# Optimization experiments

Hardware: AMD Instinct MI355X
Metric: run time of the kernel (lower is better)

Reference implementation:

```python
import jax, jax.numpy as jnp
import numpy as np
from jax import lax

N, D, K, R, T = 200000, 128, 64, 4, 50000
L = 2 * R  # positive + negative relation layers
ITERATIONS = 2


def _l2norm(x, eps=1e-12):
    # torch F.normalize(p=2): x / max(||x||, eps)
    n = jnp.sqrt(jnp.sum(x * x, axis=-1, keepdims=True))
    return x / jnp.maximum(n, eps)


def setup_inputs() -> dict:
    key = jax.random.key(0)
    ks = jax.random.split(key, 8)
    # Unique write targets (a permutation) so the last-write scatter is deterministic;
    # matches input_specs' randint intent (indices uniform in [0, N)).
    perm = jax.random.permutation(ks[0], N)
    subj_idx = perm[:T].astype(jnp.int32)
    obj_idx = perm[T:2 * T].astype(jnp.int32)
    layer_idx = jax.random.randint(ks[1], (T,), 0, L, dtype=jnp.int32)
    memberships = jax.random.randint(ks[2], (N, K), 0, 2, dtype=jnp.int32)
    embedding_m = jax.random.normal(ks[3], (N, D), dtype=jnp.float32)
    # ClassUpdate params: [d+K] -> d
    Wc = jax.random.normal(ks[4], (D + K, D), dtype=jnp.float32) / np.sqrt(D + K)
    bc = jnp.zeros((D,), dtype=jnp.float32)
    # RelationUpdate params, one layer per (relation, polarity): [2d] -> [2d]
    Wr = jax.random.normal(ks[5], (L, 2 * D, 2 * D), dtype=jnp.float32) / np.sqrt(2 * D)
    br = jnp.zeros((L, 2 * D), dtype=jnp.float32)
    return {
        'embedding_m': embedding_m,
        'memberships': memberships,
        'subj_idx': subj_idx,
        'obj_idx': obj_idx,
        'layer_idx': layer_idx,
        'Wc': Wc, 'bc': bc, 'Wr': Wr, 'br': br,
    }


def reference(embedding_m, memberships, subj_idx, obj_idx, layer_idx, Wc, bc, Wr, br):
    mem = memberships.astype(embedding_m.dtype)  # [N, K]
    t_ar = jnp.arange(T)

    def iteration(e, _):
        # --- ClassUpdate: e' = l2norm(tanh([e; m] Wc + bc)) ---
        x = jnp.concatenate([e, mem], axis=1)           # [N, d+K]
        e = _l2norm(jnp.tanh(x @ Wc + bc))              # [N, d]
        # --- RelationUpdates: reads come from the post-class-update snapshot `e`
        pair = jnp.concatenate([e[subj_idx], e[obj_idx]], axis=1)   # [T, 2d]
        # compute through all L relation layers, then select each triple's layer
        out_all = jnp.einsum('tc,lcd->tld', pair, Wr) + br          # [T, L, 2d]
        out = jnp.tanh(out_all[t_ar, layer_idx])                    # [T, 2d]
        new_s = _l2norm(out[:, :D])
        new_o = _l2norm(out[:, D:])
        e_next = e.at[subj_idx].set(new_s).at[obj_idx].set(new_o)
        return e_next, None

    e_final, _ = lax.scan(iteration, embedding_m, None, length=ITERATIONS)
    return e_final
```

## Files before the change

kernel.cpp:

```cpp
#include <hip/hip_runtime.h>
#include <hip/hip_bf16.h>


#define NROWS 200000
#define DD    128
#define KK    64
#define TT    50000
#define LL    8
#define BT    64
#define PADT  50560
#define NPASS 3125

#define NB    100
#define CHB   500
#define PL    8
#define PREPB 268
#define MBB   6250

#define WS_OFFS   0
#define WS_CNT    64
#define WS_BASE   4096
#define WS_BINS   8192
#define WS_WCP    210432
#define WS_WRP    (WS_WCP + 6*8*64*16)
#define WS_MB     (WS_WRP + 8*8*16*64*16)
#define WS_E16    (WS_MB + NROWS*8)
#define WS_NEED   (WS_E16 + (size_t)NROWS*DD*2)

typedef unsigned short u16;
typedef unsigned int   u32;
typedef unsigned long long u64;
typedef unsigned char  u8;
typedef __attribute__((ext_vector_type(8))) short bf16x8;
typedef __attribute__((ext_vector_type(4))) float f32x4;
typedef __attribute__((ext_vector_type(4))) unsigned int u32x4;

#define SWZ(row, byte) ((byte) ^ (((row)&7)<<4))

__device__ __forceinline__ u32 bfbits(float f){
  __hip_bfloat16 h = __float2bfloat16(f);
  return (u32)*reinterpret_cast<unsigned short*>(&h);
}
__device__ __forceinline__ u32 pk(float lo, float hi){
  return bfbits(lo) | (bfbits(hi) << 16);
}
__device__ __forceinline__ float qreduce16(float ss){
  ss += __shfl_xor(ss, 1, 64);
  ss += __shfl_xor(ss, 2, 64);
  ss += __shfl_xor(ss, 4, 64);
  ss += __shfl_xor(ss, 8, 64);
  return ss;
}
__device__ __forceinline__ float fast_tanh(float x){
  float a = fabsf(x);
  float e = __expf(-2.0f*a);
  float t = (1.0f - e) * __builtin_amdgcn_rcpf(1.0f + e);
  return copysignf(t, x);
}
__device__ __forceinline__ float rnorm_scale(float ss){
  return __builtin_amdgcn_rcpf(fmaxf(__builtin_amdgcn_sqrtf(ss), 1e-12f));
}
__device__ __forceinline__ void nt_store_v4(void* p, u32x4 v){
  __builtin_nontemporal_store(v, (u32x4*)p);
}

__global__ __launch_bounds__(256) void k_prep(
    const float* __restrict__ Wc, const float* __restrict__ Wr,
    uint4* __restrict__ wcp, uint4* __restrict__ wrp,
    const int* __restrict__ layer, int* __restrict__ cnt,
    const int* __restrict__ mem, u8* __restrict__ mb8)
{
  if (blockIdx.x >= PREPB + NB){
    int gid = (blockIdx.x - PREPB - NB)*256 + threadIdx.x;
    const int4* s4 = (const int4*)(mem + (size_t)gid*8);
    int4 a = s4[0], b = s4[1];
    u8 byte = (u8)((a.x!=0) | ((a.y!=0)<<1) | ((a.z!=0)<<2) | ((a.w!=0)<<3)
             | ((b.x!=0)<<4) | ((b.y!=0)<<5) | ((b.z!=0)<<6) | ((b.w!=0)<<7));
    __builtin_nontemporal_store(byte, &mb8[gid]);
    return;
  }
  if (blockIdx.x >= PREPB){
    const int bb = blockIdx.x - PREPB, lane = threadIdx.x;
    if (lane >= 64) return;
    const int lim = bb*CHB + CHB;
    int i0 = bb*CHB + lane*PL, i1 = i0 + PL; if (i1 > lim) i1 = lim;
    int c[LL] = {0,0,0,0,0,0,0,0};
    for (int i = i0; i < i1; ++i){
      int l = layer[i];
      #pragma unroll
      for (int k = 0; k < LL; ++k) c[k] += (l == k);
    }
    #pragma unroll
    for (int k = 0; k < LL; ++k){
      int v = c[k];
      v += __shfl_xor(v, 1, 64); v += __shfl_xor(v, 2, 64);
      v += __shfl_xor(v, 4, 64); v += __shfl_xor(v, 8, 64);
      v += __shfl_xor(v, 16, 64); v += __shfl_xor(v, 32, 64);
      if (lane == k) cnt[bb*LL + k] = v;
    }
    return;
  }
  int id = blockIdx.x*blockDim.x + threadIdx.x;
  if (id < 3072){
    int lane = id & 63, nt = (id >> 6) & 7, kt = id >> 9;
    int k0 = kt*32 + (lane>>4)*8, n = nt*16 + (lane&15);
    u32 p[4];
    #pragma unroll
    for (int e2 = 0; e2 < 4; ++e2)
      p[e2] = pk(Wc[(k0 + 2*e2)*DD + n], Wc[(k0 + 2*e2 + 1)*DD + n]);
    wcp[id] = make_uint4(p[0], p[1], p[2], p[3]);
  } else if (id < 3072 + 65536){
    int id2 = id - 3072;
    int lane = id2 & 63, nt = (id2>>6) & 15, kt = (id2>>10) & 7, l = id2 >> 13;
    int k0 = kt*32 + (lane>>4)*8, n = nt*16 + (lane&15);
    const float* w = Wr + (size_t)l*65536;
    u32 p[4];
    #pragma unroll
    for (int e2 = 0; e2 < 4; ++e2)
      p[e2] = pk(w[(k0 + 2*e2)*256 + n], w[(k0 + 2*e2 + 1)*256 + n]);
    wrp[id2] = make_uint4(p[0], p[1], p[2], p[3]);
  }
}

__global__ __launch_bounds__(64) void k_bin2(const int* __restrict__ cnt,
                                             int* __restrict__ offs,
                                             int* __restrict__ gbase,
                                             int* __restrict__ bins)
{
  __shared__ int pre[NB][LL];
  __shared__ int tot[LL], soffs[LL+1];
  const int t = threadIdx.x;
  if (t < LL){
    int acc = 0;
    for (int bb = 0; bb < NB; ++bb){ pre[bb][t] = acc; acc += cnt[bb*LL + t]; }
    tot[t] = acc;
  }
  __syncthreads();
  if (t == 0){
    int acc = 0;
    for (int l = 0; l < LL; ++l){
      soffs[l] = acc; offs[l] = acc;
      acc += ((tot[l] + BT - 1)/BT)*BT;
    }
    soffs[LL] = acc; offs[LL] = acc;
  }
  __syncthreads();
  for (int idx = t; idx < NB*LL; idx += 64){
    int bb = idx >> 3, k = idx & 7;
    gbase[idx] = soffs[k] + pre[bb][k];
  }
  const int k = t >> 3, sub = t & 7;
  const int sz = soffs[k+1] - soffs[k];
  for (int i = tot[k] + sub; i < sz; i += 8) bins[soffs[k] + i] = -1;
}

__global__ __launch_bounds__(64) void k_bin3(const int* __restrict__ layer,
                                             const int* __restrict__ gbase,
                                             int* __restrict__ bins)
{
  const int bb = blockIdx.x, lane = threadIdx.x;
  const int lim = bb*CHB + CHB;
  int i0 = bb*CHB + lane*PL, i1 = i0 + PL; if (i1 > lim) i1 = lim;
  int c[LL] = {0,0,0,0,0,0,0,0};
  for (int i = i0; i < i1; ++i){
    int l = layer[i];
    #pragma unroll
    for (int k = 0; k < LL; ++k) c[k] += (l == k);
  }
  int start[LL];
  #pragma unroll
  for (int k = 0; k < LL; ++k){
    int v = c[k];
    #pragma unroll
    for (int d = 1; d < 64; d <<= 1){
      int u = __shfl_up(v, d, 64);
      if (lane >= d) v += u;
    }
    start[k] = gbase[bb*LL + k] + v - c[k];
  }
  for (int i = i0; i < i1; ++i){
    int l = layer[i];
    #pragma unroll
    for (int k = 0; k < LL; ++k)
      if (l == k) bins[start[k]++] = i;
  }
}

template<bool S16, bool W16, bool WF32>
__global__ __launch_bounds__(512) void k_class(
    const float* __restrict__ srcf, const u16* __restrict__ src16,
    u16* __restrict__ e16, float* __restrict__ dstf,
    const u64* __restrict__ mbits,
    const uint4* __restrict__ wcp, const float* __restrict__ bc)
{
  __shared__ __align__(16) char smem[24576];
  __shared__ float sPart[64][9];
  __shared__ float sScale[64];
  u16* sA = (u16*)smem;

  const int tid = threadIdx.x;
  const int lane = tid & 63, wid = tid >> 6;
  const int colj = lane & 15, qw = lane >> 4;
  const int rowbase = blockIdx.x * 64;

  int crow[2], ccc[2];
  uint4  eA[2];
  float4 fA[2][2];
  #pragma unroll
  for (int v = 0; v < 2; ++v){
    int c = tid + v*512;
    crow[v] = c >> 4; ccc[v] = c & 15;
    if constexpr (S16){
      eA[v] = *(const uint4*)(src16 + (size_t)(rowbase+crow[v])*DD + ccc[v]*8);
    } else {
      const float4* s4 = (const float4*)(srcf + (size_t)(rowbase+crow[v])*DD + ccc[v]*8);
      fA[v][0] = s4[0]; fA[v][1] = s4[1];
    }
  }
  u64 mv = 0;
  if (tid < 256) mv = mbits[rowbase + (tid >> 2)];

  bf16x8 wf[6];
  #pragma unroll
  for (int kt = 0; kt < 6; ++kt)
    wf[kt] = *(const bf16x8*)&wcp[(kt*8 + wid)*64 + lane];
  const float b = bc[wid*16 + colj];

  #pragma unroll
  for (int v = 0; v < 2; ++v){
    uint4 out;
    if constexpr (S16){
      out = eA[v];
    } else {
      float4 a = fA[v][0], bb2 = fA[v][1];
      out = make_uint4(pk(a.x,a.y), pk(a.z,a.w), pk(bb2.x,bb2.y), pk(bb2.z,bb2.w));
    }
    *(uint4*)((char*)sA + crow[v]*384 + SWZ(crow[v], ccc[v]*16)) = out;
  }
  if (tid < 256){
    const int r = tid >> 2, q = tid & 3;
    u32 s = (u32)(mv >> (q*16)) & 0xFFFFu;
    u32 p[8];
    #pragma unroll
    for (int jj = 0; jj < 8; ++jj){
      u32 lo = (s >> (2*jj))     & 1u;
      u32 hi = (s >> (2*jj + 1)) & 1u;
      p[jj] = (lo ? 0x3F80u : 0u) | (hi ? 0x3F800000u : 0u);
    }
    *(uint4*)((char*)sA + r*384 + SWZ(r, 256 + q*32))      = make_uint4(p[0],p[1],p[2],p[3]);
    *(uint4*)((char*)sA + r*384 + SWZ(r, 256 + q*32 + 16)) = make_uint4(p[4],p[5],p[6],p[7]);
  }
  __syncthreads();

  f32x4 acc[4];
  #pragma unroll
  for (int m = 0; m < 4; ++m) acc[m] = (f32x4){0.f,0.f,0.f,0.f};
  #pragma unroll
  for (int m = 0; m < 4; ++m){
    int row = m*16 + colj;
    #pragma unroll
    for (int kt = 0; kt < 6; ++kt){
      bf16x8 afr = *(bf16x8*)((char*)sA + row*384 + SWZ(row, kt*64 + qw*16));
      acc[m] = __builtin_amdgcn_mfma_f32_16x16x32_bf16(afr, wf[kt], acc[m], 0,0,0);
    }
  }
  #pragma unroll
  for (int m = 0; m < 4; ++m){
    #pragma unroll
    for (int r = 0; r < 4; ++r){
      float t = fast_tanh(acc[m][r] + b);
      acc[m][r] = t;
      float ss = qreduce16(t*t);
      if (colj == 0) sPart[m*16 + qw*4 + r][wid] = ss;
    }
  }
  __syncthreads();
  if (tid < 64){
    float s = 0.f;
    #pragma unroll
    for (int i = 0; i < 8; ++i) s += sPart[tid][i];
    sScale[tid] = rnorm_scale(s);
  }
  __syncthreads();

  if constexpr (W16){
    u16* so = (u16*)smem;
    #pragma unroll
    for (int m = 0; m < 4; ++m){
      #pragma unroll
      for (int r = 0; r < 4; ++r){
        int row = m*16 + qw*4 + r;
        so[row*128 + wid*16 + colj] = (u16)bfbits(acc[m][r]*sScale[row]);
      }
    }
    __syncthreads();
    const u32x4* sp = (const u32x4*)smem;
    u32x4* gp = (u32x4*)(e16 + (size_t)rowbase*DD);
    nt_store_v4(gp + tid,       sp[tid]);
    nt_store_v4(gp + tid + 512, sp[tid + 512]);
  }
  if constexpr (WF32){
    #pragma unroll
    for (int m = 0; m < 4; ++m){
      #pragma unroll
      for (int r = 0; r < 4; ++r){
        int row = m*16 + qw*4 + r;
        dstf[(size_t)(rowbase+row)*DD + wid*16 + colj] = acc[m][r]*sScale[row];
      }
    }
  }
}

template<bool S16, bool W16, bool WF32>
__global__ __launch_bounds__(256) void k_rel(
    const float* __restrict__ ef32, u16* __restrict__ e16,
    float* __restrict__ dstf,
    const int* __restrict__ subj, const int* __restrict__ obj,
    const uint4* __restrict__ wrp, const float* __restrict__ br,
    const int* __restrict__ offs, const int* __restrict__ bins)
{
  __shared__ __align__(16) char smem[32768];
  __shared__ float sBr[256];
  __shared__ float sPart[BT][4];
  __shared__ int   sS[BT], sO[BT];
  u16* sA = (u16*)smem;

  const int tid  = threadIdx.x;
  const int base = blockIdx.x * BT;
  if (base >= offs[LL]) return;
  int l = 0;
  while (l < LL-1 && base >= offs[l+1]) ++l;

  const int lane = tid & 63, wid = tid >> 6;
  const int colj = lane & 15, qw = lane >> 4;

  const uint4* wb = wrp + (size_t)l*8192 + lane;
  bf16x8 wf[8][4];
  #pragma unroll
  for (int n = 0; n < 4; ++n){
    wf[0][n] = *(const bf16x8*)&wb[(0*16 + wid*4 + n)*64];
    wf[1][n] = *(const bf16x8*)&wb[(1*16 + wid*4 + n)*64];
  }

  sBr[tid] = br[l*256 + tid];

  const int ti = tid >> 2, q = tid & 3;
  int id = bins[base + ti];
  int rs = -1, ro = -1;
  if (id >= 0){ rs = subj[id]; ro = obj[id]; }
  if (q == 0){ sS[ti] = rs; sO[ti] = ro; }
  const int rr = (q < 2) ? rs : ro;
  if constexpr (S16){
    const u16* srcp = e16 + (size_t)rr*DD + (q & 1)*64;
    #pragma unroll
    for (int j = 0; j < 8; ++j){
      uint4 w = (id >= 0) ? ((const uint4*)srcp)[j] : make_uint4(0u,0u,0u,0u);
      *(uint4*)((char*)sA + ti*512 + SWZ(ti, q*128 + j*16)) = w;
    }
  } else {
    const float* srcp = ef32 + (size_t)rr*DD + (q & 1)*64;
    #pragma unroll
    for (int j = 0; j < 8; ++j){
      uint4 w;
      if (id >= 0){
        float4 a = ((const float4*)srcp)[2*j], b = ((const float4*)srcp)[2*j+1];
        w = make_uint4(pk(a.x,a.y), pk(a.z,a.w), pk(b.x,b.y), pk(b.z,b.w));
      } else w = make_uint4(0u,0u,0u,0u);
      *(uint4*)((char*)sA + ti*512 + SWZ(ti, q*128 + j*16)) = w;
    }
  }
  __syncthreads();

  f32x4 acc[4][4];
  #pragma unroll
  for (int m = 0; m < 4; ++m)
    #pragma unroll
    for (int n = 0; n < 4; ++n) acc[m][n] = (f32x4){0.f,0.f,0.f,0.f};

  #pragma unroll
  for (int kt = 0; kt < 8; ++kt){
    if (kt + 2 < 8){
      #pragma unroll
      for (int n = 0; n < 4; ++n)
        wf[kt+2][n] = *(const bf16x8*)&wb[((kt+2)*16 + wid*4 + n)*64];
    }
    #pragma unroll
    for (int m = 0; m < 4; ++m){
      int row = m*16 + colj;
      bf16x8 afr = *(bf16x8*)((char*)sA + row*512 + SWZ(row, kt*64 + qw*16));
      #pragma unroll
      for (int n = 0; n < 4; ++n)
        acc[m][n] = __builtin_amdgcn_mfma_f32_16x16x32_bf16(afr, wf[kt][n], acc[m][n], 0,0,0);
    }
  }

  #pragma unroll
  for (int m = 0; m < 4; ++m){
    #pragma unroll
    for (int n = 0; n < 4; ++n){
      float b = sBr[(wid*4 + n)*16 + colj];
      #pragma unroll
      for (int r = 0; r < 4; ++r)
        acc[m][n][r] = fast_tanh(acc[m][n][r] + b);
    }
    #pragma unroll
    for (int r = 0; r < 4; ++r){
      float ss = acc[m][0][r]*acc[m][0][r] + acc[m][1][r]*acc[m][1][r]
               + acc[m][2][r]*acc[m][2][r] + acc[m][3][r]*acc[m][3][r];
      ss = qreduce16(ss);
      if (colj == 0) sPart[m*16 + qw*4 + r][wid] = ss;
    }
  }
  __syncthreads();

  const int h = wid >> 1;
  if constexpr (W16){
    #pragma unroll
    for (int m = 0; m < 4; ++m){
      #pragma unroll
      for (int r = 0; r < 4; ++r){
        int tri = m*16 + qw*4 + r;
        float ss = sPart[tri][2*h] + sPart[tri][2*h + 1];
        float sc = rnorm_scale(ss);
        #pragma unroll
        for (int n = 0; n < 4; ++n){
          int col = (wid*4 + n)*16 + colj;
          float v = acc[m][n][r]*sc;
          *(u16*)((char*)smem + tri*512 + ((col*2) ^ ((tri&7)<<4))) = (u16)bfbits(v);
        }
      }
    }
    __syncthreads();
    #pragma unroll
    for (int k = 0; k < 8; ++k){
      int c = tid + k*256;
      int tri = c >> 5, hh = (c >> 4) & 1, sub = c & 15;
      int row = hh ? sO[tri] : sS[tri];
      if (row >= 0){
        u32x4 v = *(const u32x4*)((char*)smem + ((c*16) ^ ((tri&7)<<4)));
        nt_store_v4((u32x4*)(e16 + (size_t)row*DD) + sub, v);
      }
    }
  }
  if constexpr (WF32){
    #pragma unroll
    for (int m = 0; m < 4; ++m){
      #pragma unroll
      for (int r = 0; r < 4; ++r){
        int tri = m*16 + qw*4 + r;
        int row = h ? sO[tri] : sS[tri];
        if (row < 0) continue;
        float ss = sPart[tri][2*h] + sPart[tri][2*h + 1];
        float sc = rnorm_scale(ss);
        #pragma unroll
        for (int n = 0; n < 4; ++n){
          int cc = (wid*4 + n)*16 + colj - h*DD;
          dstf[(size_t)row*DD + cc] = acc[m][n][r]*sc;
        }
      }
    }
  }
}

extern "C" void kernel_launch(void* const* d_in, const int* in_sizes, int n_in,
                              void* d_out, int out_size, void* d_ws, size_t ws_size,
                              hipStream_t stream) {
  (void)in_sizes; (void)n_in; (void)out_size;
  const float* emb  = (const float*)d_in[0];
  const int*   mem  = (const int*)  d_in[1];
  const int*   subj = (const int*)  d_in[2];
  const int*   obj  = (const int*)  d_in[3];
  const int*   lay  = (const int*)  d_in[4];
  const float* Wc   = (const float*)d_in[5];
  const float* bc   = (const float*)d_in[6];
  const float* Wr   = (const float*)d_in[7];
  const float* br   = (const float*)d_in[8];

  float* e   = (float*)d_out;
  char*  wsb = (char*)d_ws;
  int*   offs  = (int*)(wsb + WS_OFFS);
  int*   cnt   = (int*)(wsb + WS_CNT);
  int*   gbase = (int*)(wsb + WS_BASE);
  int*   bins  = (int*)(wsb + WS_BINS);
  uint4* wcp   = (uint4*)(wsb + WS_WCP);
  uint4* wrp   = (uint4*)(wsb + WS_WRP);
  u64*   mbits = (u64*)(wsb + WS_MB);
  u8*    mb8   = (u8*)(wsb + WS_MB);
  u16*   e16   = (u16*)(wsb + WS_E16);

  k_prep<<<PREPB + NB + MBB, 256, 0, stream>>>(Wc, Wr, wcp, wrp, lay, cnt, mem, mb8);
  k_bin2<<<1, 64, 0, stream>>>(cnt, offs, gbase, bins);
  k_bin3<<<NB, 64, 0, stream>>>(lay, gbase, bins);

  if (ws_size >= WS_NEED){
    k_class<false,true,false><<<NPASS, 512, 0, stream>>>(
        emb, nullptr, e16, nullptr, mbits, wcp, bc);
    k_rel<true,true,false><<<PADT/BT, 256, 0, stream>>>(
        nullptr, e16, nullptr, subj, obj, wrp, br, offs, bins);
    k_class<true,false,true><<<NPASS, 512, 0, stream>>>(
        nullptr, e16, nullptr, e, mbits, wcp, bc);
    k_rel<false,false,true><<<PADT/BT, 256, 0, stream>>>(
        e, nullptr, e, subj, obj, wrp, br, offs, bins);
  } else {
    k_class<false,false,true><<<NPASS, 512, 0, stream>>>(
        emb, nullptr, nullptr, e, mbits, wcp, bc);
    k_rel<false,false,true><<<PADT/BT, 256, 0, stream>>>(
        e, nullptr, e, subj, obj, wrp, br, offs, bins);
    k_class<false,false,true><<<NPASS, 512, 0, stream>>>(
        e, nullptr, nullptr, e, mbits, wcp, bc);
    k_rel<false,false,true><<<PADT/BT, 256, 0, stream>>>(
        e, nullptr, e, subj, obj, wrp, br, offs, bins);
  }
}
```

Before: 174.6 us.

## Use persistent double-buffered class-update kernel with async LDS loads

Replaces the class-update kernel on the full-workspace path with a persistent 1024-block kernel. It keeps Wc fragments in registers and double-buffers 64-row bf16 tiles into LDS through global_load_lds, so loads overlap the MFMA work. The fp32 embedding is converted to bf16 in the prep kernel, so the first class pass reads bf16 instead of fp32. The cost is an extra conversion pass over the embedding, and the in-place e16 read/write relies on each block owning its own tiles.

Result: slower. 213.7 us (+22.4%).

```diff
diff --git a/kernel.cpp b/kernel.cpp
--- a/kernel.cpp
+++ b/kernel.cpp
@@ -10,12 +10,14 @@
 #define BT    64
 #define PADT  50560
 #define NPASS 3125
+#define CGRID 1024
 
 #define NB    100
 #define CHB   500
 #define PL    8
 #define PREPB 268
 #define MBB   6250
+#define ECVB  12500
 
 #define WS_OFFS   0
 #define WS_CNT    64
@@ -63,13 +65,28 @@
 __device__ __forceinline__ void nt_store_v4(void* p, u32x4 v){
   __builtin_nontemporal_store(v, (u32x4*)p);
 }
+__device__ __forceinline__ void gload16(const void* g, void* l){
+  __builtin_amdgcn_global_load_lds(
+      (const __attribute__((address_space(1))) void*)g,
+      (__attribute__((address_space(3))) void*)l, 16, 0, 0);
+}
 
 __global__ __launch_bounds__(256) void k_prep(
     const float* __restrict__ Wc, const float* __restrict__ Wr,
     uint4* __restrict__ wcp, uint4* __restrict__ wrp,
     const int* __restrict__ layer, int* __restrict__ cnt,
-    const int* __restrict__ mem, u8* __restrict__ mb8)
+    const int* __restrict__ mem, u8* __restrict__ mb8,
+    const float* __restrict__ emb, u16* __restrict__ e16)
 {
+  if (blockIdx.x >= PREPB + NB + MBB){
+    size_t gid = (size_t)(blockIdx.x - PREPB - NB - MBB)*256 + threadIdx.x;
+    const float4* s4 = (const float4*)(emb + gid*8);
+    float4 a = s4[0], b = s4[1];
+    u32x4 o;
+    o.x = pk(a.x,a.y); o.y = pk(a.z,a.w); o.z = pk(b.x,b.y); o.w = pk(b.z,b.w);
+    nt_store_v4(e16 + gid*8, o);
+    return;
+  }
   if (blockIdx.x >= PREPB + NB){
     int gid = (blockIdx.x - PREPB - NB)*256 + threadIdx.x;
     const int4* s4 = (const int4*)(mem + (size_t)gid*8);
@@ -186,8 +203,146 @@
   }
 }
 
+template<bool W16, bool WF32>
+__global__ __launch_bounds__(256) void k_class_p(
+    const u16* __restrict__ src16, u16* __restrict__ e16out,
+    float* __restrict__ dstf, const u64* __restrict__ mbits,
+    const uint4* __restrict__ wcp, const float* __restrict__ bc)
+{
+  __shared__ __align__(16) u16 sE[2][8192];
+  __shared__ __align__(16) u16 sM[2][4096];
+  __shared__ float sPart[64][4];
+
+  const int tid = threadIdx.x;
+  const int lane = tid & 63, wid = tid >> 6;
+  const int colj = lane & 15, qw = lane >> 4;
+  const int mrow = tid >> 2, mq = tid & 3;
+
+  bf16x8 wf[6][2];
+  #pragma unroll
+  for (int kt = 0; kt < 6; ++kt)
+    #pragma unroll
+    for (int j = 0; j < 2; ++j)
+      wf[kt][j] = *(const bf16x8*)&wcp[(kt*8 + 2*wid + j)*64 + lane];
+  const float b0 = bc[(2*wid)*16 + colj];
+  const float b1 = bc[(2*wid+1)*16 + colj];
+
+  auto issue = [&](int buf, int tile){
+    #pragma unroll
+    for (int i = 0; i < 4; ++i){
+      int p   = wid*4096 + i*1024 + lane*16;
+      int row = p >> 8;
+      int cG  = ((p >> 4) & 15) ^ (row & 7);
+      const u16* g = src16 + (((size_t)tile*64 + row) << 7) + cG*8;
+      gload16(g, (void*)&sE[buf][(wid*4096 + i*1024) >> 1]);
+    }
+  };
+
+  int t = blockIdx.x;
+  int cur = 0;
+  issue(0, t);
+  u64 mv = mbits[(size_t)t*64 + mrow];
+
+  for (;;){
+    {
+      u32 s = (u32)(mv >> (mq*16)) & 0xFFFFu;
+      u32 p[8];
+      #pragma unroll
+      for (int jj = 0; jj < 8; ++jj){
+        u32 lo = (s >> (2*jj))     & 1u;
+        u32 hi = (s >> (2*jj + 1)) & 1u;
+        p[jj] = (lo ? 0x3F80u : 0u) | (hi ? 0x3F800000u : 0u);
+      }
+      int c0 = (mq*2)     ^ (mrow & 7);
+      int c1 = (mq*2 + 1) ^ (mrow & 7);
+      *(uint4*)&sM[cur][mrow*64 + c0*8] = make_uint4(p[0],p[1],p[2],p[3]);
+      *(uint4*)&sM[cur][mrow*64 + c1*8] = make_uint4(p[4],p[5],p[6],p[7]);
+    }
+    __syncthreads();
+
+    const int tn = t + CGRID;
+    const bool more = (tn < NPASS);
+    if (more){
+      issue(cur ^ 1, tn);
+      mv = mbits[(size_t)tn*64 + mrow];
+    }
+
+    f32x4 acc[4][2];
+    #pragma unroll
+    for (int m = 0; m < 4; ++m){
+      acc[m][0] = (f32x4){0.f,0.f,0.f,0.f};
+      acc[m][1] = (f32x4){0.f,0.f,0.f,0.f};
+    }
+    #pragma unroll
+    for (int m = 0; m < 4; ++m){
+      const int row = m*16 + colj;
+      #pragma unroll
+      for (int kt = 0; kt < 4; ++kt){
+        bf16x8 afr = *(bf16x8*)&sE[cur][row*128 + (((kt*4+qw) ^ (row&7))*8)];
+        acc[m][0] = __builtin_amdgcn_mfma_f32_16x16x32_bf16(afr, wf[kt][0], acc[m][0], 0,0,0);
+        acc[m][1] = __builtin_amdgcn_mfma_f32_16x16x32_bf16(afr, wf[kt][1], acc[m][1], 0,0,0);
+      }
+      #pragma unroll
+      for (int kt = 4; kt < 6; ++kt){
+        bf16x8 afr = *(bf16x8*)&sM[cur][row*64 + ((((kt-4)*4+qw) ^ (row&7))*8)];
+        acc[m][0] = __builtin_amdgcn_mfma_f32_16x16x32_bf16(afr, wf[kt][0], acc[m][0], 0,0,0);
+        acc[m][1] = __builtin_amdgcn_mfma_f32_16x16x32_bf16(afr, wf[kt][1], acc[m][1], 0,0,0);
+      }
+    }
+    #pragma unroll
+    for (int m = 0; m < 4; ++m){
+      #pragma unroll
+      for (int r = 0; r < 4; ++r){
+        float t0 = fast_tanh(acc[m][0][r] + b0);
+        float t1 = fast_tanh(acc[m][1][r] + b1);
+        acc[m][0][r] = t0; acc[m][1][r] = t1;
+        float ss = qreduce16(t0*t0 + t1*t1);
+        if (colj == 0) sPart[m*16 + qw*4 + r][wid] = ss;
+      }
+    }
+    __syncthreads();
+
+    const size_t rowbase = (size_t)t*64;
+    if constexpr (W16){
+      u16* so = sE[cur];
+      #pragma unroll
+      for (int m = 0; m < 4; ++m){
+        #pragma unroll
+        for (int r = 0; r < 4; ++r){
+          int row = m*16 + qw*4 + r;
+          f32x4 p = *(f32x4*)sPart[row];
+          float sc = rnorm_scale(p[0] + p[1] + p[2] + p[3]);
+          so[row*128 + (2*wid)*16 + colj]      = (u16)bfbits(acc[m][0][r]*sc);
+          so[row*128 + (2*wid+1)*16 + colj]    = (u16)bfbits(acc[m][1][r]*sc);
+        }
+      }
+      __syncthreads();
+      #pragma unroll
+      for (int k = 0; k < 4; ++k){
+        int c = tid + k*256;
+        nt_store_v4((void*)(e16out + rowbase*DD + c*8), *(const u32x4*)&so[c*8]);
+      }
+    }
+    if constexpr (WF32){
+      #pragma unroll
+      for (int m = 0; m < 4; ++m){
+        #pragma unroll
+        for (int r = 0; r < 4; ++r){
+          int row = m*16 + qw*4 + r;
+          f32x4 p = *(f32x4*)sPart[row];
+          float sc = rnorm_scale(p[0] + p[1] + p[2] + p[3]);
+          dstf[(rowbase+row)*DD + (2*wid)*16 + colj]   = acc[m][0][r]*sc;
+          dstf[(rowbase+row)*DD + (2*wid+1)*16 + colj] = acc[m][1][r]*sc;
+        }
+      }
+    }
+    if (!more) break;
+    t = tn; cur ^= 1;
+  }
+}
+
 template<bool S16, bool W16, bool WF32>
-__global__ __launch_bounds__(512) void k_class(
+__global__ __launch_bounds__(512) void k_class_fb(
     const float* __restrict__ srcf, const u16* __restrict__ src16,
     u16* __restrict__ e16, float* __restrict__ dstf,
     const u64* __restrict__ mbits,
@@ -488,25 +643,27 @@
   u8*    mb8   = (u8*)(wsb + WS_MB);
   u16*   e16   = (u16*)(wsb + WS_E16);
 
-  k_prep<<<PREPB + NB + MBB, 256, 0, stream>>>(Wc, Wr, wcp, wrp, lay, cnt, mem, mb8);
+  const bool full = (ws_size >= WS_NEED);
+  const int prep_grid = PREPB + NB + MBB + (full ? ECVB : 0);
+  k_prep<<<prep_grid, 256, 0, stream>>>(Wc, Wr, wcp, wrp, lay, cnt, mem, mb8, emb, e16);
   k_bin2<<<1, 64, 0, stream>>>(cnt, offs, gbase, bins);
   k_bin3<<<NB, 64, 0, stream>>>(lay, gbase, bins);
 
-  if (ws_size >= WS_NEED){
-    k_class<false,true,false><<<NPASS, 512, 0, stream>>>(
-        emb, nullptr, e16, nullptr, mbits, wcp, bc);
+  if (full){
+    k_class_p<true,false><<<CGRID, 256, 0, stream>>>(
+        e16, e16, nullptr, mbits, wcp, bc);
     k_rel<true,true,false><<<PADT/BT, 256, 0, stream>>>(
         nullptr, e16, nullptr, subj, obj, wrp, br, offs, bins);
-    k_class<true,false,true><<<NPASS, 512, 0, stream>>>(
-        nullptr, e16, nullptr, e, mbits, wcp, bc);
+    k_class_p<false,true><<<CGRID, 256, 0, stream>>>(
+        e16, nullptr, e, mbits, wcp, bc);
     k_rel<false,false,true><<<PADT/BT, 256, 0, stream>>>(
         e, nullptr, e, subj, obj, wrp, br, offs, bins);
   } else {
-    k_class<false,false,true><<<NPASS, 512, 0, stream>>>(
+    k_class_fb<false,false,true><<<NPASS, 512, 0, stream>>>(
         emb, nullptr, nullptr, e, mbits, wcp, bc);
     k_rel<false,false,true><<<PADT/BT, 256, 0, stream>>>(
         e, nullptr, e, subj, obj, wrp, br, offs, bins);
-    k_class<false,false,true><<<NPASS, 512, 0, stream>>>(
+    k_class_fb<false,false,true><<<NPASS, 512, 0, stream>>>(
         e, nullptr, nullptr, e, mbits, wcp, bc);
     k_rel<false,false,true><<<PADT/BT, 256, 0, stream>>>(
         e, nullptr, e, subj, obj, wrp, br, offs, bins);
```
